# Kernel tuning notes

Hardware: AMD Instinct MI355X
Metric: run time of the kernel (lower is better)

## Reference

```python
import jax, jax.numpy as jnp
import numpy as np

W_BIT = 4
OUT_F = 11008
IN_F = 4096
K = 16
TOKENS = 2048


def unpack_sign(qweight, out_f, in_f):
    """qweight: [w_bit, out_f*in_f//8] ints in [0,256). Each byte packs 8 signs,
    LSB-first: bit j of byte m -> element m*8+j; bit 1 -> +1, bit 0 -> -1.
    Returns float32 signs of shape [w_bit, out_f, in_f]."""
    shifts = jnp.arange(8, dtype=qweight.dtype)
    bits = (qweight[..., None] >> shifts) & 1  # [w_bit, n_bytes, 8]
    sign = (2 * bits - 1).astype(jnp.float32)
    return sign.reshape(qweight.shape[0], out_f, in_f)


def setup_inputs() -> dict:
    key = jax.random.key(0)
    k1, k2, k3, k4 = jax.random.split(key, 4)
    x = jax.random.normal(k1, (TOKENS, IN_F), dtype=jnp.float32)
    qweight = jax.random.randint(k2, (W_BIT, OUT_F * IN_F // 8), 0, 256, dtype=jnp.int32)
    u = jax.random.normal(k3, (W_BIT, OUT_F, K), dtype=jnp.float32) * 0.05
    vt = jax.random.normal(k4, (W_BIT, K, IN_F), dtype=jnp.float32) * 0.05
    return {"x": x, "qweight": qweight, "u": u, "vt": vt}


def reference(x, qweight, u, vt):
    # Reconstruct w = sum_i sign_i * (u_i @ vt_i), then y = x @ w.T  (forward_l0)
    sign = unpack_sign(qweight, OUT_F, IN_F)                  # [b, O, I]
    low_rank = jnp.einsum('bok,bki->boi', u, vt)              # [b, O, I]
    w = jnp.sum(sign * low_rank, axis=0)                      # [O, I]
    return x @ w.T                                            # [T, O]
```

## Files before the change

### kernel.cpp

```cpp
#include <hip/hip_runtime.h>
#include <cstdint>
#include <cstddef>

#define TOKENS 2048
#define IN_F   4096
#define OUT_F  11008
#define W_BIT  4
#define RANK   16
#define QWB    (OUT_F * IN_F / 8)

typedef unsigned short ushort_t;
typedef __attribute__((ext_vector_type(8))) short   short8;
typedef __attribute__((ext_vector_type(4))) float   floatx4;

__device__ __forceinline__ ushort_t f2bf(float f) {
  union { float f; uint32_t u; } c; c.f = f;
  uint32_t r = c.u + 0x7FFFu + ((c.u >> 16) & 1u);
  return (ushort_t)(r >> 16);
}

__device__ __forceinline__ void gl_lds16(const void* g, void* l) {
  __builtin_amdgcn_global_load_lds(
      (const __attribute__((address_space(1))) uint32_t*)g,
      (__attribute__((address_space(3))) uint32_t*)l, 16, 0, 0);
}

__global__ __launch_bounds__(256) void k_cvt_x(const float* __restrict__ x,
                                               ushort_t* __restrict__ xb) {
  int idx = blockIdx.x * 256 + threadIdx.x;
  float4 v = ((const float4*)x)[idx];
  ushort4 r;
  r.x = f2bf(v.x); r.y = f2bf(v.y); r.z = f2bf(v.z); r.w = f2bf(v.w);
  ((ushort4*)xb)[idx] = r;
}

#define N_U  (W_BIT * OUT_F * RANK)
#define N_VT (W_BIT * RANK * IN_F)
__global__ __launch_bounds__(256) void k_prep_uv(const float* __restrict__ u,
                                                 const float* __restrict__ vt,
                                                 ushort_t* __restrict__ ub,
                                                 ushort_t* __restrict__ vtT) {
  int idx = blockIdx.x * 256 + threadIdx.x;
  if (idx < N_U) {
    ub[idx] = f2bf(u[idx]);
  } else {
    int e = idx - N_U;
    int b = e >> 16;
    int r = e & 65535;
    int k = r >> 12;
    int i = r & 4095;
    vtT[((size_t)b * IN_F + i) * RANK + k] = f2bf(vt[e]);
  }
}

__global__ __launch_bounds__(256) void k_build_w(const int* __restrict__ qw,
                                                 const ushort_t* __restrict__ ub,
                                                 const ushort_t* __restrict__ vtT,
                                                 ushort_t* __restrict__ w) {
  __shared__ int qs[W_BIT * 128 * 20];
  const int tid = threadIdx.x;
  const int ob = blockIdx.x / (IN_F / 128);
  const int ib = blockIdx.x % (IN_F / 128);
  const int o0 = ob * 128, i0 = ib * 128;
  const int lane = tid & 63, wv = tid >> 6;
  const int wm = (wv >> 1) * 64, wn = (wv & 1) * 64;
  const int l16 = lane & 15, q = lane >> 4;
  const bool qlo = (q < 2);
  const int koff = (q & 1) * 8;
  const short8 zf = (short8)0;

  #pragma unroll
  for (int n = 0; n < 8; ++n) {
    int c = n * 256 + tid;
    int b = c >> 9, rem = c & 511;
    int row = rem >> 2, part = rem & 3;
    int4 v = *(const int4*)(qw + (size_t)b * QWB +
                            (size_t)(o0 + row) * (IN_F / 8) + (i0 >> 3) + part * 4);
    *(int4*)&qs[(b * 128 + row) * 20 + part * 4] = v;
  }

  floatx4 acc[16];
  #pragma unroll
  for (int i = 0; i < 16; ++i) acc[i] = (floatx4){0.f, 0.f, 0.f, 0.f};

  const int qc_base = (wn >> 3) + (l16 >> 3);
  const int bit = l16 & 7;

  __syncthreads();

  #pragma unroll
  for (int b = 0; b < W_BIT; ++b) {
    short8 af[4], bfr[4];
    #pragma unroll
    for (int mi = 0; mi < 4; ++mi) {
      short8 v = *(const short8*)&ub[((size_t)b * OUT_F + o0 + wm + mi * 16 + l16) * RANK + koff];
      af[mi] = qlo ? v : zf;
    }
    #pragma unroll
    for (int ni = 0; ni < 4; ++ni) {
      short8 v = *(const short8*)&vtT[((size_t)b * IN_F + i0 + wn + ni * 16 + l16) * RANK + koff];
      bfr[ni] = qlo ? v : zf;
    }

    #pragma unroll
    for (int mi = 0; mi < 4; ++mi) {
      floatx4 p[4];
      #pragma unroll
      for (int ni = 0; ni < 4; ++ni)
        p[ni] = __builtin_amdgcn_mfma_f32_16x16x32_bf16(
            af[mi], bfr[ni], (floatx4){0.f, 0.f, 0.f, 0.f}, 0, 0, 0);
      #pragma unroll
      for (int v4 = 0; v4 < 4; ++v4) {
        const int o_loc = wm + mi * 16 + q * 4 + v4;
        const int* qrow = &qs[(b * 128 + o_loc) * 20];
        #pragma unroll
        for (int ni = 0; ni < 4; ++ni) {
          int qv = qrow[qc_base + ni * 2];
          float pv = p[ni][v4];
          acc[mi * 4 + ni][v4] += ((qv >> bit) & 1) ? pv : -pv;
        }
      }
    }
  }

  #pragma unroll
  for (int mi = 0; mi < 4; ++mi) {
    #pragma unroll
    for (int v4 = 0; v4 < 4; ++v4) {
      const int o = o0 + wm + mi * 16 + q * 4 + v4;
      #pragma unroll
      for (int ni = 0; ni < 4; ++ni)
        w[(size_t)o * IN_F + i0 + wn + ni * 16 + l16] = f2bf(acc[mi * 4 + ni][v4]);
    }
  }
}

#define NSTEP (IN_F / 32)
#define SLOT  16384
#define NSLOT 4
__global__ __launch_bounds__(256) void k_gemm_bt(const ushort_t* __restrict__ A,
                                                 const ushort_t* __restrict__ B,
                                                 float* __restrict__ C) {
  __shared__ __attribute__((aligned(16))) char lds[NSLOT * SLOT];
  const int tid = threadIdx.x;
  const int wg = (blockIdx.x & 7) * 172 + (blockIdx.x >> 3);
  const int bm = wg & 15;
  const int bn = wg >> 4;
  const int lane = tid & 63, wv = tid >> 6;
  const int wm = wv >> 1, wn = wv & 1;
  const int l16 = lane & 15, q = lane >> 4;
  const int sQ = q ^ ((l16 >> 1) & 3);

  const size_t ar = (size_t)bm * 128, br = (size_t)bn * 128;
  const int qsrc = (tid & 3) ^ ((tid >> 3) & 3);
  const ushort_t* Ae = A + (ar + (tid >> 2)) * IN_F + qsrc * 8;
  const ushort_t* Be = B + (br + (tid >> 2)) * IN_F + qsrc * 8;
  const int ldsoff = (tid & 192) * 16;
  const int aFrag = (wm * 64 + l16) * 64 + sQ * 16;
  const int bFrag = (wn * 64 + l16) * 64 + sQ * 16;

  floatx4 acc[4][4];
  #pragma unroll
  for (int mi = 0; mi < 4; ++mi)
    #pragma unroll
    for (int ni = 0; ni < 4; ++ni) acc[mi][ni] = (floatx4){0.f, 0.f, 0.f, 0.f};

  short8 fa0[4], fb0[4], fa1[4], fb1[4];
  int sLd = SLOT;
  int sWr = 3 * SLOT;

#define STAGEK(kt, off) do {                                                 \
    const size_t _k0 = (size_t)(kt) * 32;                                    \
    char* _d = lds + (off) + ldsoff;                                         \
    gl_lds16(Ae + _k0,                _d);                                   \
    gl_lds16(Ae + 64 * IN_F + _k0,    _d + 4096);                            \
    gl_lds16(Be + _k0,                _d + 8192);                            \
    gl_lds16(Be + 64 * IN_F + _k0,    _d + 12288);                           \
  } while (0)

#define LDFR(FA, FB, off) do {                                               \
    const char* _ab = lds + (off);                                           \
    const char* _bb = _ab + 8192;                                            \
    _Pragma("unroll") for (int mi = 0; mi < 4; ++mi)                         \
      FA[mi] = *(const short8*)(_ab + aFrag + mi * 1024);                    \
    _Pragma("unroll") for (int ni = 0; ni < 4; ++ni)                         \
      FB[ni] = *(const short8*)(_bb + bFrag + ni * 1024);                    \
  } while (0)

#define MFMA16(MA, MB) do {                                                  \
    __builtin_amdgcn_s_setprio(1);                                           \
    _Pragma("unroll") for (int mi = 0; mi < 4; ++mi)                         \
      _Pragma("unroll") for (int ni = 0; ni < 4; ++ni)                       \
        acc[mi][ni] = __builtin_amdgcn_mfma_f32_16x16x32_bf16(               \
            MA[mi], MB[ni], acc[mi][ni], 0, 0, 0);                           \
    __builtin_amdgcn_s_setprio(0);                                           \
  } while (0)

#define PHASE(u_, VM, DO_STAGE, FA, FB, MA, MB) do {                         \
    asm volatile(VM ::: "memory");                                           \
    __builtin_amdgcn_s_barrier();                                            \
    asm volatile("" ::: "memory");                                           \
    LDFR(FA, FB, sLd);                      \
    if (DO_STAGE) STAGEK((u_) + 3, sWr);                                     \
    MFMA16(MA, MB);                        \
    sLd += SLOT; if (sLd == NSLOT * SLOT) sLd = 0;                           \
    sWr += SLOT; if (sWr == NSLOT * SLOT) sWr = 0;                           \
  } while (0)

  STAGEK(0, 0); STAGEK(1, SLOT); STAGEK(2, 2 * SLOT);
  asm volatile("s_waitcnt vmcnt(8)" ::: "memory");
  __builtin_amdgcn_s_barrier();
  asm volatile("" ::: "memory");
  LDFR(fa0, fb0, 0);

  for (int u = 0; u < NSTEP - 4; u += 2) {
    PHASE(u,     "s_waitcnt vmcnt(4)", true, fa1, fb1, fa0, fb0);
    PHASE(u + 1, "s_waitcnt vmcnt(4)", true, fa0, fb0, fa1, fb1);
  }
  PHASE(NSTEP - 4, "s_waitcnt vmcnt(4)", true,  fa1, fb1, fa0, fb0);
  PHASE(NSTEP - 3, "s_waitcnt vmcnt(4)", false, fa0, fb0, fa1, fb1);
  PHASE(NSTEP - 2, "s_waitcnt vmcnt(0)", false, fa1, fb1, fa0, fb0);
  MFMA16(fa1, fb1);

#undef STAGEK
#undef LDFR
#undef MFMA16
#undef PHASE

  #pragma unroll
  for (int mi = 0; mi < 4; ++mi) {
    #pragma unroll
    for (int ni = 0; ni < 4; ++ni) {
      #pragma unroll
      for (int v = 0; v < 4; ++v) {
        int r = bm * 128 + wm * 64 + mi * 16 + q * 4 + v;
        int c = bn * 128 + wn * 64 + ni * 16 + l16;
        C[(size_t)r * OUT_F + c] = acc[mi][ni][v];
      }
    }
  }
}

extern "C" void kernel_launch(void* const* d_in, const int* in_sizes, int n_in,
                              void* d_out, int out_size, void* d_ws, size_t ws_size,
                              hipStream_t stream) {
  (void)in_sizes; (void)n_in; (void)out_size; (void)ws_size;
  const float* x  = (const float*)d_in[0];
  const int*   qw = (const int*)d_in[1];
  const float* u  = (const float*)d_in[2];
  const float* vt = (const float*)d_in[3];
  float* out = (float*)d_out;

  char* wsp = (char*)d_ws;
  ushort_t* xb  = (ushort_t*)wsp;
  ushort_t* wb  = (ushort_t*)(wsp + (size_t)TOKENS * IN_F * 2);
  ushort_t* ubf = (ushort_t*)(wsp + (size_t)TOKENS * IN_F * 2 + (size_t)OUT_F * IN_F * 2);
  ushort_t* vtT = (ushort_t*)(wsp + (size_t)TOKENS * IN_F * 2 + (size_t)OUT_F * IN_F * 2 +
                              (size_t)N_U * 2);

  k_cvt_x<<<TOKENS * IN_F / 1024, 256, 0, stream>>>(x, xb);
  k_prep_uv<<<(N_U + N_VT) / 256, 256, 0, stream>>>(u, vt, ubf, vtT);
  k_build_w<<<(OUT_F / 128) * (IN_F / 128), 256, 0, stream>>>(qw, ubf, vtT, wb);
  k_gemm_bt<<<16 * (OUT_F / 128), 256, 0, stream>>>(xb, wb, out);
}
```

Measured before the change: 448.2 us.

## Enlarge GEMM tile to 256x128 with triple-buffered LDS pipeline

```diff
diff --git a/kernel.cpp b/kernel.cpp
--- a/kernel.cpp
+++ b/kernel.cpp
@@ -136,104 +136,90 @@
 }
 
 #define NSTEP (IN_F / 32)
-#define SLOT  16384
-#define NSLOT 4
-__global__ __launch_bounds__(256) void k_gemm_bt(const ushort_t* __restrict__ A,
-                                                 const ushort_t* __restrict__ B,
-                                                 float* __restrict__ C) {
+#define SLOT  24576
+#define NSLOT 3
+__global__ __launch_bounds__(256, 2) void k_gemm_bt(const ushort_t* __restrict__ A,
+                                                    const ushort_t* __restrict__ B,
+                                                    float* __restrict__ C) {
   __shared__ __attribute__((aligned(16))) char lds[NSLOT * SLOT];
   const int tid = threadIdx.x;
-  const int wg = (blockIdx.x & 7) * 172 + (blockIdx.x >> 3);
-  const int bm = wg & 15;
-  const int bn = wg >> 4;
+  const int wg = (blockIdx.x & 7) * 86 + (blockIdx.x >> 3);
+  const int bm = wg & 7;
+  const int bn = wg >> 3;
   const int lane = tid & 63, wv = tid >> 6;
   const int wm = wv >> 1, wn = wv & 1;
   const int l16 = lane & 15, q = lane >> 4;
   const int sQ = q ^ ((l16 >> 1) & 3);
 
-  const size_t ar = (size_t)bm * 128, br = (size_t)bn * 128;
+  const size_t ar = (size_t)bm * 256, br = (size_t)bn * 128;
   const int qsrc = (tid & 3) ^ ((tid >> 3) & 3);
   const ushort_t* Ae = A + (ar + (tid >> 2)) * IN_F + qsrc * 8;
   const ushort_t* Be = B + (br + (tid >> 2)) * IN_F + qsrc * 8;
   const int ldsoff = (tid & 192) * 16;
-  const int aFrag = (wm * 64 + l16) * 64 + sQ * 16;
+  const int aFrag = (wm * 128 + l16) * 64 + sQ * 16;
   const int bFrag = (wn * 64 + l16) * 64 + sQ * 16;
 
-  floatx4 acc[4][4];
-  #pragma unroll
-  for (int mi = 0; mi < 4; ++mi)
+  floatx4 acc[8][4];
+  #pragma unroll
+  for (int mi = 0; mi < 8; ++mi)
     #pragma unroll
     for (int ni = 0; ni < 4; ++ni) acc[mi][ni] = (floatx4){0.f, 0.f, 0.f, 0.f};
 
-  short8 fa0[4], fb0[4], fa1[4], fb1[4];
-  int sLd = SLOT;
-  int sWr = 3 * SLOT;
+  short8 af[8], bf[4];
+  int sLd = 0;
+  int sWr = 2 * SLOT;
 
 #define STAGEK(kt, off) do {                                                 \
     const size_t _k0 = (size_t)(kt) * 32;                                    \
     char* _d = lds + (off) + ldsoff;                                         \
-    gl_lds16(Ae + _k0,                _d);                                   \
-    gl_lds16(Ae + 64 * IN_F + _k0,    _d + 4096);                            \
-    gl_lds16(Be + _k0,                _d + 8192);                            \
-    gl_lds16(Be + 64 * IN_F + _k0,    _d + 12288);                           \
+    gl_lds16(Ae + _k0,                 _d);                                  \
+    gl_lds16(Ae +  64 * IN_F + _k0,    _d + 4096);                           \
+    gl_lds16(Ae + 128 * IN_F + _k0,    _d + 8192);                           \
+    gl_lds16(Ae + 192 * IN_F + _k0,    _d + 12288);                          \
+    gl_lds16(Be + _k0,                 _d + 16384);                          \
+    gl_lds16(Be +  64 * IN_F + _k0,    _d + 20480);                          \
   } while (0)
 
-#define LDFR(FA, FB, off) do {                                               \
-    const char* _ab = lds + (off);                                           \
-    const char* _bb = _ab + 8192;                                            \
-    _Pragma("unroll") for (int mi = 0; mi < 4; ++mi)                         \
-      FA[mi] = *(const short8*)(_ab + aFrag + mi * 1024);                    \
-    _Pragma("unroll") for (int ni = 0; ni < 4; ++ni)                         \
-      FB[ni] = *(const short8*)(_bb + bFrag + ni * 1024);                    \
-  } while (0)
-
-#define MFMA16(MA, MB) do {                                                  \
-    __builtin_amdgcn_s_setprio(1);                                           \
-    _Pragma("unroll") for (int mi = 0; mi < 4; ++mi)                         \
-      _Pragma("unroll") for (int ni = 0; ni < 4; ++ni)                       \
-        acc[mi][ni] = __builtin_amdgcn_mfma_f32_16x16x32_bf16(               \
-            MA[mi], MB[ni], acc[mi][ni], 0, 0, 0);                           \
-    __builtin_amdgcn_s_setprio(0);                                           \
-  } while (0)
-
-#define PHASE(u_, VM, DO_STAGE, FA, FB, MA, MB) do {                         \
+#define PHASE(u_, VM, DO_STAGE) do {                                         \
     asm volatile(VM ::: "memory");                                           \
     __builtin_amdgcn_s_barrier();                                            \
     asm volatile("" ::: "memory");                                           \
-    LDFR(FA, FB, sLd);                      \
-    if (DO_STAGE) STAGEK((u_) + 3, sWr);                                     \
-    MFMA16(MA, MB);                        \
+    {                                                                        \
+      const char* _ab = lds + sLd;                                           \
+      const char* _bb = _ab + 16384;                                         \
+      _Pragma("unroll") for (int mi = 0; mi < 8; ++mi)                       \
+        af[mi] = *(const short8*)(_ab + aFrag + mi * 1024);                  \
+      _Pragma("unroll") for (int ni = 0; ni < 4; ++ni)                       \
+        bf[ni] = *(const short8*)(_bb + bFrag + ni * 1024);                  \
+    }                                                                        \
+    if (DO_STAGE) STAGEK((u_) + 2, sWr);                                     \
+    __builtin_amdgcn_s_setprio(1);                                           \
+    _Pragma("unroll") for (int mi = 0; mi < 8; ++mi)                         \
+      _Pragma("unroll") for (int ni = 0; ni < 4; ++ni)                       \
+        acc[mi][ni] = __builtin_amdgcn_mfma_f32_16x16x32_bf16(               \
+            af[mi], bf[ni], acc[mi][ni], 0, 0, 0);                           \
+    __builtin_amdgcn_s_setprio(0);                                           \
     sLd += SLOT; if (sLd == NSLOT * SLOT) sLd = 0;                           \
     sWr += SLOT; if (sWr == NSLOT * SLOT) sWr = 0;                           \
   } while (0)
 
-  STAGEK(0, 0); STAGEK(1, SLOT); STAGEK(2, 2 * SLOT);
-  asm volatile("s_waitcnt vmcnt(8)" ::: "memory");
-  __builtin_amdgcn_s_barrier();
-  asm volatile("" ::: "memory");
-  LDFR(fa0, fb0, 0);
-
-  for (int u = 0; u < NSTEP - 4; u += 2) {
-    PHASE(u,     "s_waitcnt vmcnt(4)", true, fa1, fb1, fa0, fb0);
-    PHASE(u + 1, "s_waitcnt vmcnt(4)", true, fa0, fb0, fa1, fb1);
-  }
-  PHASE(NSTEP - 4, "s_waitcnt vmcnt(4)", true,  fa1, fb1, fa0, fb0);
-  PHASE(NSTEP - 3, "s_waitcnt vmcnt(4)", false, fa0, fb0, fa1, fb1);
-  PHASE(NSTEP - 2, "s_waitcnt vmcnt(0)", false, fa1, fb1, fa0, fb0);
-  MFMA16(fa1, fb1);
+  STAGEK(0, 0); STAGEK(1, SLOT);
+
+  for (int u = 0; u < NSTEP - 2; ++u)
+    PHASE(u, "s_waitcnt vmcnt(6)", true);
+  PHASE(NSTEP - 2, "s_waitcnt vmcnt(6)", false);
+  PHASE(NSTEP - 1, "s_waitcnt vmcnt(0)", false);
 
 #undef STAGEK
-#undef LDFR
-#undef MFMA16
 #undef PHASE
 
   #pragma unroll
-  for (int mi = 0; mi < 4; ++mi) {
+  for (int mi = 0; mi < 8; ++mi) {
     #pragma unroll
     for (int ni = 0; ni < 4; ++ni) {
       #pragma unroll
       for (int v = 0; v < 4; ++v) {
-        int r = bm * 128 + wm * 64 + mi * 16 + q * 4 + v;
+        int r = bm * 256 + wm * 128 + mi * 16 + q * 4 + v;
         int c = bn * 128 + wn * 64 + ni * 16 + l16;
         C[(size_t)r * OUT_F + c] = acc[mi][ni][v];
       }
@@ -261,5 +247,5 @@
   k_cvt_x<<<TOKENS * IN_F / 1024, 256, 0, stream>>>(x, xb);
   k_prep_uv<<<(N_U + N_VT) / 256, 256, 0, stream>>>(u, vt, ubf, vtT);
   k_build_w<<<(OUT_F / 128) * (IN_F / 128), 256, 0, stream>>>(qw, ubf, vtT, wb);
-  k_gemm_bt<<<16 * (OUT_F / 128), 256, 0, stream>>>(xb, wb, out);
-}
+  k_gemm_bt<<<8 * (OUT_F / 128), 256, 0, stream>>>(xb, wb, out);
+}
```

Result: faster. 422.1 us (-5.8%).
